# Optimization experiments

Measured on AMD Instinct MI355X. Metric: run time of the kernel, lower is better.

Reference implementation:

```python
import jax, jax.numpy as jnp
import numpy as np

EPS = 1e-12
H = 256
W = 256
RANK = 4
CTX = 1024
BATCH = 32
FF = (H + W) * RANK * 4  # 8192
STD = 0.001


def _norm(x, axis):
    # torch: (x - mean) / sqrt(var(unbiased) + eps)
    m = jnp.mean(x, axis=axis, keepdims=True)
    v = jnp.var(x, axis=axis, keepdims=True, ddof=1)
    return (x - m) / jnp.sqrt(v + EPS)


def _norm_polar(x):
    # x: [B, N, 2]; magnitude-normalize relative to per-batch max magnitude
    x_abs = jnp.sqrt(x[..., 0] ** 2 + x[..., 1] ** 2 + EPS)          # [B, N]
    h = x_abs / (jnp.max(x_abs, axis=-1, keepdims=True) + EPS)       # [B, N]
    xn = x / (x_abs[..., None] + EPS)                                # [B, N, 2]
    return jnp.stack([h * xn[..., 0], h * xn[..., 1]], axis=-1)


def setup_inputs() -> dict:
    key = jax.random.key(0)
    ks = jax.random.split(key, 12)

    def lin(k, fan_in, shape):
        b = 1.0 / np.sqrt(fan_in)
        return jax.random.uniform(k, shape, jnp.float32, -b, b)

    weights_static = jnp.concatenate([
        jax.random.normal(ks[9], (1, H, W, 2), jnp.float32) * STD,
        jax.random.normal(ks[10], (1, H, W, 2), jnp.float32) * STD
        + jnp.array([1.0, 0.0], jnp.float32),
    ], axis=0)  # [2, H, W, 2]

    return {
        "x": jax.random.normal(ks[0], (BATCH, CTX), jnp.float32),
        "W_in": lin(ks[1], CTX, (FF, CTX)),
        "b_in": lin(ks[2], CTX, (FF,)),
        "W_gate": lin(ks[3], CTX, (FF, CTX)),
        "b_gate": lin(ks[4], CTX, (FF,)),
        "W_t": lin(ks[5], FF, (FF, FF)),
        "b_t": lin(ks[6], FF, (FF,)),
        "conv_w": lin(ks[7], RANK, (RANK, RANK)),  # 1x1 conv kernel [out, in]
        "conv_b": lin(ks[8], RANK, (RANK,)),
        "weights_static": weights_static,
        "weights_mod": jax.random.normal(ks[11], (4, H, W), jnp.float32) * STD,
    }


def reference(x, W_in, b_in, W_gate, b_gate, W_t, b_t, conv_w, conv_b,
              weights_static, weights_mod):
    b = x.shape[0]
    # dual linear projections (dropout p=0 -> identity)
    xt = x @ W_in.T + b_in            # [B, FF]
    xg = x @ W_gate.T + b_gate        # [B, FF]
    stack = jnp.stack([xt, xg], axis=0).reshape(2, b, 4, -1)
    stack = _norm(stack, -1)
    ctx = (stack[0] * jnp.tanh(stack[1])).reshape(b, -1)   # gated, [B, FF]
    ctx = ctx @ W_t.T + b_t                                 # [B, FF]
    ctx = ctx.reshape(b, 4, RANK, H + W)
    modc = _norm(ctx, -1)
    # outer product -> [B, 4, RANK, H, W]
    mod = jnp.tanh(jnp.einsum('bkri,bkrj->bkrij', modc[..., :H], modc[..., H:]))
    # channel 0: 1x1 conv over rank channels, then sum channels (keepdim)
    mod_real = jnp.einsum('oi,bihw->bohw', conv_w, mod[:, 0]) + conv_b[None, :, None, None]
    mod_real = jnp.sum(mod_real, axis=1, keepdims=True)     # [B, 1, H, W]
    mod_other = jnp.sum(mod[:, 1:], axis=2)                 # [B, 3, H, W]
    mod = jnp.concatenate([mod_real, mod_other], axis=1)    # [B, 4, H, W]
    mod = weights_mod[None] * mod

    A0 = weights_static[0]            # [H, W, 2]
    A1 = weights_static[1]            # [H, W, 2]
    Bm = jnp.moveaxis(mod[:, 0:2], 1, -1)                   # [B, H, W, 2]
    ms_r = A1[..., 0] * Bm[..., 0] - A1[..., 1] * Bm[..., 1]
    ms_i = A1[..., 0] * Bm[..., 1] - A1[..., 1] * Bm[..., 0]
    mod_scaled = jnp.stack([ms_r, ms_i], axis=-1)           # [B, H, W, 2]
    mod_scaled = _norm_polar(mod_scaled.reshape(b, H * W, 2)).reshape(b, H, W, 2)

    mag = jnp.sqrt(mod_scaled[..., 0] ** 2 + mod_scaled[..., 1] ** 2 + EPS)
    mag = jnp.sqrt(jnp.mean(mag, axis=(-1, -2)) + EPS)      # [B]
    mod_scaled = mod_scaled / mag[:, None, None, None]

    mod_weights = A0[None] + mod_scaled                     # [B, H, W, 2]

    mod_proj = jnp.moveaxis(mod[:, 2:], 1, -1)              # [B, H, W, 2]
    mod_proj = _norm_polar(mod_proj.reshape(b, H * W, 2)).reshape(b, H, W, 2)
    den = jnp.sqrt(mod_proj[..., 0] ** 2 + mod_proj[..., 1] ** 2 + EPS)
    theta_cos = mod_proj[..., 0] / den
    theta_sin = mod_proj[..., 1] / den
    weights = mod_weights[..., 0] * theta_cos + mod_weights[..., 1] * theta_sin
    return weights  # [B, H, W]
```

## Files before the change

### kernel.cpp

```cpp
#include <hip/hip_runtime.h>
#include <cstddef>

#define NB   32
#define CTXD 1024
#define FFD  8192
#define HD   256
#define WD   256
#define NPIX 65536
#define EPSF 1e-12f

typedef __attribute__((ext_vector_type(8))) short bf16x8;
typedef __attribute__((ext_vector_type(4))) float f32x4;


__device__ __forceinline__ float ftanh(float x){
  float ax = fabsf(x);
  float e  = __expf(2.0f*ax);
  float r  = 1.0f - 2.0f*__builtin_amdgcn_rcpf(e + 1.0f);
  return copysignf(r, x);
}

__device__ __forceinline__ unsigned short f2bf(float f){
  unsigned u = __float_as_uint(f);
  unsigned r = (u + 0x7FFFu + ((u >> 16) & 1u)) >> 16;
  return (unsigned short)r;
}
__device__ __forceinline__ float bf2f(unsigned short s){
  return __uint_as_float((unsigned)s << 16);
}

__device__ __forceinline__ void split3(float f, unsigned short& s0,
                                       unsigned short& s1, unsigned short& s2){
  s0 = f2bf(f);
  float r1 = f - bf2f(s0);
  s1 = f2bf(r1);
  float r2 = r1 - bf2f(s1);
  s2 = f2bf(r2);
}

__device__ __forceinline__ void block_reduce4(float& a, float& b, float& c, float& d){
  for (int off = 32; off > 0; off >>= 1){
    a += __shfl_down(a, off); b += __shfl_down(b, off);
    c += __shfl_down(c, off); d += __shfl_down(d, off);
  }
  __shared__ float lds[16];
  int wid = threadIdx.x >> 6, lane = threadIdx.x & 63;
  if (lane == 0){ lds[wid*4+0]=a; lds[wid*4+1]=b; lds[wid*4+2]=c; lds[wid*4+3]=d; }
  __syncthreads();
  a = (lds[0]+lds[4])+(lds[8]+lds[12]);
  b = (lds[1]+lds[5])+(lds[9]+lds[13]);
  c = (lds[2]+lds[6])+(lds[10]+lds[14]);
  d = (lds[3]+lds[7])+(lds[11]+lds[15]);
}

__device__ __forceinline__ void pixel_core(
    const float* __restrict__ lds, int h, int w, int pix,
    float cw0, float cw1, float cw2, float cw3, float cb,
    const float* __restrict__ wmod, const float* __restrict__ wstat,
    float& r_, float& i_, float& p_, float& q_){
  float sk[4];
  #pragma unroll
  for (int k = 0; k < 4; ++k){
    float acc = 0.f;
    #pragma unroll
    for (int r = 0; r < 4; ++r){
      int kr = k*4 + r;
      float u  = lds[kr*512 + h];
      float vv = lds[kr*512 + 256 + w];
      float tt = ftanh(u*vv);
      float cwr = (r==0)?cw0:(r==1)?cw1:(r==2)?cw2:cw3;
      acc += (k==0) ? cwr*tt : tt;
    }
    sk[k] = acc;
  }
  sk[0] += cb;
  float m0 = sk[0]*wmod[0*NPIX+pix];
  float m1 = sk[1]*wmod[1*NPIX+pix];
  float m2 = sk[2]*wmod[2*NPIX+pix];
  float m3 = sk[3]*wmod[3*NPIX+pix];
  float2 A1 = *(const float2*)(wstat + (size_t)(NPIX + pix)*2);
  r_ = A1.x*m0 - A1.y*m1;
  i_ = A1.x*m1 - A1.y*m0;
  p_ = m2; q_ = m3;
}


__global__ __launch_bounds__(256) void k_prep(
    const float* __restrict__ x, unsigned short* __restrict__ P,
    float* __restrict__ red){
  int g = blockIdx.x*256 + threadIdx.x;
  if (g < 64) red[g] = 0.0f;
  int b = g >> 7, grp = g & 127;
  int koff = grp*8;
  int c = grp >> 2, kg = grp & 3;
  const float* src = x + (size_t)b*CTXD + koff;
  float4 v0 = *(const float4*)(src), v1 = *(const float4*)(src+4);
  float vv[8] = {v0.x,v0.y,v0.z,v0.w,v1.x,v1.y,v1.z,v1.w};
  bf16x8 a0, a1, a2;
  #pragma unroll
  for (int e = 0; e < 8; ++e){
    unsigned short s0,s1,s2; split3(vv[e],s0,s1,s2);
    a0[e]=(short)s0; a1[e]=(short)s1; a2[e]=(short)s2;
  }
  size_t base = (size_t)c*3072 + (b>>4)*512 + kg*128 + (b&15)*8;
  *(bf16x8*)(P + base)        = a0;
  *(bf16x8*)(P + base + 1024) = a1;
  *(bf16x8*)(P + base + 2048) = a2;
}

template<int KC>
__global__ __launch_bounds__(256) void k_gemm_mfma(
    const float* __restrict__ W0, const float* __restrict__ W1,
    const unsigned short* __restrict__ BP,
    float* __restrict__ Cp, int K, size_t zstride){
  const float* __restrict__ W = blockIdx.z ? W1 : W0;
  int wave = threadIdx.x >> 6;
  int lane = threadIdx.x & 63;
  int f0   = blockIdx.x*64 + wave*16;
  int kc   = blockIdx.y;
  int row  = lane & 15;
  int kg   = lane >> 4;
  int rot  = blockIdx.x & (KC-1);
  const float* Wb = W + (size_t)(f0+row)*K + kc*KC*32 + kg*8;
  const unsigned short* Bb = BP + (size_t)kc*KC*3072 + kg*128 + row*8;
  f32x4 acc0={0.f,0.f,0.f,0.f}, acc1={0.f,0.f,0.f,0.f};
  const float* wp = Wb + rot*32;
  float4 w0 = *(const float4*)(wp), w1 = *(const float4*)(wp+4);
  for (int c = 0; c < KC; ++c){
    int rc = (c + rot) & (KC-1);
    const unsigned short* bp = Bb + (size_t)rc*3072;
    bf16x8 b0h0 = *(const bf16x8*)(bp);
    bf16x8 b0h1 = *(const bf16x8*)(bp +  512);
    bf16x8 b1h0 = *(const bf16x8*)(bp + 1024);
    bf16x8 b1h1 = *(const bf16x8*)(bp + 1536);
    bf16x8 b2h0 = *(const bf16x8*)(bp + 2048);
    bf16x8 b2h1 = *(const bf16x8*)(bp + 2560);
    float4 cw0 = w0, cw1 = w1;
    if (c + 1 < KC){
      int rn = (c + 1 + rot) & (KC-1);
      wp = Wb + rn*32;
      w0 = *(const float4*)(wp); w1 = *(const float4*)(wp+4);
    }
    bf16x8 a0, a1, a2;
    float wv[8] = {cw0.x,cw0.y,cw0.z,cw0.w,cw1.x,cw1.y,cw1.z,cw1.w};
    #pragma unroll
    for (int e = 0; e < 8; ++e){
      unsigned short s0,s1,s2; split3(wv[e],s0,s1,s2);
      a0[e]=(short)s0; a1[e]=(short)s1; a2[e]=(short)s2;
    }
    acc0 = __builtin_amdgcn_mfma_f32_16x16x32_bf16(a0, b0h0, acc0, 0,0,0);
    acc1 = __builtin_amdgcn_mfma_f32_16x16x32_bf16(a0, b0h1, acc1, 0,0,0);
    acc0 = __builtin_amdgcn_mfma_f32_16x16x32_bf16(a0, b1h0, acc0, 0,0,0);
    acc1 = __builtin_amdgcn_mfma_f32_16x16x32_bf16(a0, b1h1, acc1, 0,0,0);
    acc0 = __builtin_amdgcn_mfma_f32_16x16x32_bf16(a1, b0h0, acc0, 0,0,0);
    acc1 = __builtin_amdgcn_mfma_f32_16x16x32_bf16(a1, b0h1, acc1, 0,0,0);
    acc0 = __builtin_amdgcn_mfma_f32_16x16x32_bf16(a0, b2h0, acc0, 0,0,0);
    acc1 = __builtin_amdgcn_mfma_f32_16x16x32_bf16(a0, b2h1, acc1, 0,0,0);
    acc0 = __builtin_amdgcn_mfma_f32_16x16x32_bf16(a1, b1h0, acc0, 0,0,0);
    acc1 = __builtin_amdgcn_mfma_f32_16x16x32_bf16(a1, b1h1, acc1, 0,0,0);
    acc0 = __builtin_amdgcn_mfma_f32_16x16x32_bf16(a2, b0h0, acc0, 0,0,0);
    acc1 = __builtin_amdgcn_mfma_f32_16x16x32_bf16(a2, b0h1, acc1, 0,0,0);
  }
  float* __restrict__ C = Cp + (size_t)blockIdx.z*zstride + (size_t)kc*(FFD*32);
  #pragma unroll
  for (int r = 0; r < 4; ++r){
    int f = f0 + kg*4 + r;
    C[(size_t)f*32 + row]      = acc0[r];
    C[(size_t)f*32 + 16 + row] = acc1[r];
  }
}

__global__ __launch_bounds__(256) void k_reduce1(
    const float* __restrict__ Cp, const float* __restrict__ bin,
    const float* __restrict__ bg, float* __restrict__ xtT,
    float* __restrict__ xgT){
  int g = blockIdx.x*256 + threadIdx.x;
  int m = g >> 18, idx = g & 262143;
  int f = idx >> 5;
  const float* __restrict__ cp = Cp + (size_t)m*(8ull*FFD*32);
  float s = (m ? bg : bin)[f];
  #pragma unroll
  for (int sI = 0; sI < 8; ++sI) s += cp[(size_t)sI*(FFD*32) + idx];
  (m ? xgT : xtT)[idx] = s;
}

__global__ __launch_bounds__(256) void k_reduce2(
    const float* __restrict__ Cp, const float* __restrict__ bias,
    float* __restrict__ outT){
  int g = blockIdx.x*256 + threadIdx.x;
  int f = g >> 5;
  float s = bias[f];
  #pragma unroll
  for (int sI = 0; sI < 16; ++sI) s += Cp[(size_t)sI*(FFD*32) + g];
  outT[g] = s;
}

__global__ __launch_bounds__(256) void k_normgate(
    const float* __restrict__ xtT, const float* __restrict__ xgT,
    unsigned short* __restrict__ P){
  int b = blockIdx.x >> 2, g4 = blockIdx.x & 3;
  int t = threadIdx.x;
  int f8 = g4*2048 + t*8;
  float vt[8], vg[8];
  float st=0.f, sst=0.f, sg=0.f, ssg=0.f;
  #pragma unroll
  for (int i = 0; i < 8; ++i){
    int f = f8 + i;
    float a = xtT[(size_t)f*NB + b];
    float c = xgT[(size_t)f*NB + b];
    vt[i]=a; vg[i]=c;
    st += a; sst += a*a; sg += c; ssg += c*c;
  }
  block_reduce4(st, sst, sg, ssg);
  float mt = st * (1.0f/2048.0f);
  float it = rsqrtf((sst - st*mt) * (1.0f/2047.0f) + EPSF);
  float mg = sg * (1.0f/2048.0f);
  float ig = rsqrtf((ssg - sg*mg) * (1.0f/2047.0f) + EPSF);
  bf16x8 a0, a1, a2;
  #pragma unroll
  for (int i = 0; i < 8; ++i){
    float nt = (vt[i]-mt)*it;
    float ng = (vg[i]-mg)*ig;
    float cv = nt * ftanh(ng);
    unsigned short s0,s1,s2; split3(cv,s0,s1,s2);
    a0[i]=(short)s0; a1[i]=(short)s1; a2[i]=(short)s2;
  }
  int c2 = f8 >> 5, kg = (f8 >> 3) & 3;
  size_t base = (size_t)c2*3072 + (b>>4)*512 + kg*128 + (b&15)*8;
  *(bf16x8*)(P + base)        = a0;
  *(bf16x8*)(P + base + 1024) = a1;
  *(bf16x8*)(P + base + 2048) = a2;
}

__global__ __launch_bounds__(256) void k_norm512(
    const float* __restrict__ ctx2T, float* __restrict__ modc){
  int b = blockIdx.x >> 4, kr = blockIdx.x & 15;
  int t = threadIdx.x;
  int base = kr*512;
  float v0 = ctx2T[(base + t      )*NB + b];
  float v1 = ctx2T[(base + 256 + t)*NB + b];
  float s = v0+v1, ss = v0*v0 + v1*v1, d0=0.f, d1=0.f;
  block_reduce4(s, ss, d0, d1);
  float m   = s * (1.0f/512.0f);
  float inv = rsqrtf((ss - s*m) * (1.0f/511.0f) + EPSF);
  modc[b*FFD + base + t      ] = (v0-m)*inv;
  modc[b*FFD + base + 256 + t] = (v1-m)*inv;
}

__global__ __launch_bounds__(256) void k_scan(
    const float* __restrict__ modc,
    const float* __restrict__ convw, const float* __restrict__ convb,
    const float* __restrict__ wmod, const float* __restrict__ wstat,
    float* __restrict__ red, float* __restrict__ magpart){
  int b = blockIdx.x >> 4, chunk = blockIdx.x & 15;
  int t = threadIdx.x;
  __shared__ float lds[16*512];
  #pragma unroll
  for (int i = 0; i < 8; ++i){
    float4 v = *(const float4*)(modc + (size_t)b*FFD + (i*256 + t)*4);
    *(float4*)(lds + (i*256 + t)*4) = v;
  }
  float cw0 = convw[0]+convw[4]+convw[8]+convw[12];
  float cw1 = convw[1]+convw[5]+convw[9]+convw[13];
  float cw2 = convw[2]+convw[6]+convw[10]+convw[14];
  float cw3 = convw[3]+convw[7]+convw[11]+convw[15];
  float cb  = convb[0]+convb[1]+convb[2]+convb[3];
  __syncthreads();
  int w = t;
  float mxs = 0.f, mxp = 0.f, sas = 0.f;
  for (int it = 0; it < 16; ++it){
    int h = chunk*16 + it;
    int pix = h*WD + w;
    float r_, i_, p_, q_;
    pixel_core(lds, h, w, pix, cw0, cw1, cw2, cw3, cb, wmod, wstat,
               r_, i_, p_, q_);
    float as = sqrtf(r_*r_ + i_*i_ + EPSF);
    float ap = sqrtf(p_*p_ + q_*q_ + EPSF);
    mxs = fmaxf(mxs, as); mxp = fmaxf(mxp, ap);
    sas += as;
  }
  for (int off = 32; off > 0; off >>= 1){
    mxs = fmaxf(mxs, __shfl_down(mxs, off));
    mxp = fmaxf(mxp, __shfl_down(mxp, off));
    sas += __shfl_down(sas, off);
  }
  __shared__ float lred[12];
  int wid = t >> 6, lane = t & 63;
  if (lane == 0){ lred[wid] = mxs; lred[4+wid] = mxp; lred[8+wid] = sas; }
  __syncthreads();
  if (t == 0){
    float a = fmaxf(fmaxf(lred[0],lred[1]), fmaxf(lred[2],lred[3]));
    float p = fmaxf(fmaxf(lred[4],lred[5]), fmaxf(lred[6],lred[7]));
    float s = (lred[8]+lred[9])+(lred[10]+lred[11]);
    atomicMax((int*)&red[b],    __float_as_int(a));
    atomicMax((int*)&red[32+b], __float_as_int(p));
    magpart[b*16 + chunk] = s;
  }
}

__global__ __launch_bounds__(256) void k_final(
    const float* __restrict__ modc,
    const float* __restrict__ convw, const float* __restrict__ convb,
    const float* __restrict__ wmod, const float* __restrict__ wstat,
    const float* __restrict__ red, const float* __restrict__ magpart,
    float* __restrict__ out){
  int b = blockIdx.x >> 4, chunk = blockIdx.x & 15;
  int t = threadIdx.x;
  __shared__ float lds[16*512];
  __shared__ float s_im;
  if (t < 16){
    float v = magpart[b*16 + t];
    for (int off = 8; off > 0; off >>= 1) v += __shfl_down(v, off);
    if (t == 0){
      float maxs = red[b];
      s_im = rsqrtf(v*(1.0f/65536.0f)/(maxs + EPSF) + EPSF);
    }
  }
  #pragma unroll
  for (int i = 0; i < 8; ++i){
    float4 v = *(const float4*)(modc + (size_t)b*FFD + (i*256 + t)*4);
    *(float4*)(lds + (i*256 + t)*4) = v;
  }
  float cw0 = convw[0]+convw[4]+convw[8]+convw[12];
  float cw1 = convw[1]+convw[5]+convw[9]+convw[13];
  float cw2 = convw[2]+convw[6]+convw[10]+convw[14];
  float cw3 = convw[3]+convw[7]+convw[11]+convw[15];
  float cb  = convb[0]+convb[1]+convb[2]+convb[3];
  __syncthreads();
  float im = s_im;
  float maxs = red[b], maxp = red[32+b];
  int w = t;
  for (int it = 0; it < 16; ++it){
    int h = chunk*16 + it;
    int pix = h*WD + w;
    float r_, i_, p_, q_;
    pixel_core(lds, h, w, pix, cw0, cw1, cw2, cw3, cb, wmod, wstat,
               r_, i_, p_, q_);
    float as = sqrtf(r_*r_ + i_*i_ + EPSF);
    float fs = (as/(maxs+EPSF))/(as+EPSF)*im;
    float2 A0 = *(const float2*)(wstat + (size_t)pix*2);
    float mwr = A0.x + fs*r_;
    float mwi = A0.y + fs*i_;
    float ap = sqrtf(p_*p_ + q_*q_ + EPSF);
    float fp = (ap/(maxp+EPSF))/(ap+EPSF);
    float mpr = fp*p_, mpi = fp*q_;
    float den = sqrtf(mpr*mpr + mpi*mpi + EPSF);
    out[(size_t)b*NPIX + pix] = (mwr*mpr + mwi*mpi)/den;
  }
}


extern "C" void kernel_launch(void* const* d_in, const int* in_sizes, int n_in,
                              void* d_out, int out_size, void* d_ws, size_t ws_size,
                              hipStream_t stream){
  const float* x     = (const float*)d_in[0];
  const float* Win   = (const float*)d_in[1];
  const float* bin   = (const float*)d_in[2];
  const float* Wg    = (const float*)d_in[3];
  const float* bg    = (const float*)d_in[4];
  const float* Wt    = (const float*)d_in[5];
  const float* bt    = (const float*)d_in[6];
  const float* convw = (const float*)d_in[7];
  const float* convb = (const float*)d_in[8];
  const float* wstat = (const float*)d_in[9];
  const float* wmod  = (const float*)d_in[10];
  float* out = (float*)d_out;
  float* ws  = (float*)d_ws;

  float* xtT   = ws;
  float* xgT   = ws + 262144;
  float* ctx2T = ws;
  float* modc  = ws + 262144;
  unsigned short* P2 = (unsigned short*)(ws + 524288);
  unsigned short* P1 = (unsigned short*)(ws + 917504);
  float* Cp    = ws + 966656;
  float* red     = ws + 5160960;
  float* magpart = ws + 5161024;

  k_prep<<<16, 256, 0, stream>>>(x, P1, red);
  k_gemm_mfma<4><<<dim3(128,8,2), 256, 0, stream>>>(Win, Wg, P1,
                                                    Cp, CTXD, 8ull*FFD*32);
  k_reduce1<<<2048, 256, 0, stream>>>(Cp, bin, bg, xtT, xgT);
  k_normgate<<<128, 256, 0, stream>>>(xtT, xgT, P2);
  k_gemm_mfma<16><<<dim3(128,16,1), 256, 0, stream>>>(Wt, Wt, P2,
                                                      Cp, FFD, 0);
  k_reduce2<<<1024, 256, 0, stream>>>(Cp, bt, ctx2T);
  k_norm512<<<512, 256, 0, stream>>>(ctx2T, modc);
  k_scan<<<512, 256, 0, stream>>>(modc, convw, convb, wmod, wstat, red, magpart);
  k_final<<<512, 256, 0, stream>>>(modc, convw, convb, wmod, wstat, red,
                                   magpart, out);
}
```

Before: 174.0 us.

## Stage W_t tiles via async global-to-LDS loads with double buffering

Replaces the direct-load MFMA GEMM for the large FFxFF projection with a new kernel. It streams 64x64 fp32 weight tiles into shared memory using the global_load_lds builtin, double-buffered so the next tile loads while the current one is split into three bf16 parts and fed to MFMA. The K-step order is rotated per block so neighbouring blocks read different column slices at the same time. This aims to hide DRAM latency on the bandwidth-bound weight stream, at the cost of 32KB of LDS per block and a barrier every step.

New measurement: 163.5 us. 6.0% less time.

```diff
diff --git a/kernel.cpp b/kernel.cpp
--- a/kernel.cpp
+++ b/kernel.cpp
@@ -36,6 +36,12 @@
   s1 = f2bf(r1);
   float r2 = r1 - bf2f(s1);
   s2 = f2bf(r2);
+}
+
+__device__ __forceinline__ void gload_lds16(const float* g, float* l){
+  __builtin_amdgcn_global_load_lds(
+      (__attribute__((address_space(1))) void*)const_cast<float*>(g),
+      (__attribute__((address_space(3))) void*)l, 16, 0, 0);
 }
 
 __device__ __forceinline__ void block_reduce4(float& a, float& b, float& c, float& d){
@@ -170,6 +176,94 @@
   }
 }
 
+template<int STEPS>
+__global__ __launch_bounds__(256) void k_gemm_lds(
+    const float* __restrict__ W, const unsigned short* __restrict__ BP,
+    float* __restrict__ Cp, int K){
+  __shared__ float tile[2][4096];
+  const int t    = threadIdx.x;
+  const int wv   = t >> 6, lane = t & 63;
+  const int f0   = blockIdx.x * 64;
+  const int kc   = blockIdx.y;
+  const int row  = lane & 15, kg = lane >> 4;
+  const int srot = blockIdx.x & (STEPS - 1);
+  const size_t kslice = (size_t)kc * STEPS * 64;
+
+  f32x4 acc0 = {0.f,0.f,0.f,0.f}, acc1 = {0.f,0.f,0.f,0.f};
+
+  auto stage = [&](int buf, int s){
+    const size_t kbase = kslice + (size_t)s*64;
+    #pragma unroll
+    for (int i = 0; i < 4; ++i){
+      int r = wv*16 + i*4 + (lane >> 4);
+      const float* gsrc = W + (size_t)(f0 + r)*K + kbase + (lane & 15)*4;
+      gload_lds16(gsrc, &tile[buf][(wv*16 + i*4)*64]);
+    }
+  };
+
+  int cur = 0;
+  stage(0, srot);
+  __syncthreads();
+
+  for (int s = 0; s < STEPS; ++s){
+    const int sc = (s + srot) & (STEPS - 1);
+    const int k0 = kc*STEPS*2 + sc*2;
+    const unsigned short* bp0 = BP + (size_t)k0*3072     + kg*128 + row*8;
+    const unsigned short* bp1 = BP + (size_t)(k0+1)*3072 + kg*128 + row*8;
+    bf16x8 c0b0h0 = *(const bf16x8*)(bp0);
+    bf16x8 c0b0h1 = *(const bf16x8*)(bp0 +  512);
+    bf16x8 c0b1h0 = *(const bf16x8*)(bp0 + 1024);
+    bf16x8 c0b1h1 = *(const bf16x8*)(bp0 + 1536);
+    bf16x8 c0b2h0 = *(const bf16x8*)(bp0 + 2048);
+    bf16x8 c0b2h1 = *(const bf16x8*)(bp0 + 2560);
+    bf16x8 c1b0h0 = *(const bf16x8*)(bp1);
+    bf16x8 c1b0h1 = *(const bf16x8*)(bp1 +  512);
+    bf16x8 c1b1h0 = *(const bf16x8*)(bp1 + 1024);
+    bf16x8 c1b1h1 = *(const bf16x8*)(bp1 + 1536);
+    bf16x8 c1b2h0 = *(const bf16x8*)(bp1 + 2048);
+    bf16x8 c1b2h1 = *(const bf16x8*)(bp1 + 2560);
+    if (s + 1 < STEPS) stage(cur ^ 1, (s + 1 + srot) & (STEPS - 1));
+    #pragma unroll
+    for (int c = 0; c < 2; ++c){
+      const float* wp = &tile[cur][(wv*16 + row)*64 + c*32 + kg*8];
+      float4 w0 = *(const float4*)(wp);
+      float4 w1 = *(const float4*)(wp + 4);
+      bf16x8 a0, a1, a2;
+      float wv8[8] = {w0.x,w0.y,w0.z,w0.w,w1.x,w1.y,w1.z,w1.w};
+      #pragma unroll
+      for (int e = 0; e < 8; ++e){
+        unsigned short s0,s1,s2; split3(wv8[e],s0,s1,s2);
+        a0[e]=(short)s0; a1[e]=(short)s1; a2[e]=(short)s2;
+      }
+      bf16x8 b0h0 = c ? c1b0h0 : c0b0h0, b0h1 = c ? c1b0h1 : c0b0h1;
+      bf16x8 b1h0 = c ? c1b1h0 : c0b1h0, b1h1 = c ? c1b1h1 : c0b1h1;
+      bf16x8 b2h0 = c ? c1b2h0 : c0b2h0, b2h1 = c ? c1b2h1 : c0b2h1;
+      acc0 = __builtin_amdgcn_mfma_f32_16x16x32_bf16(a0, b0h0, acc0, 0,0,0);
+      acc1 = __builtin_amdgcn_mfma_f32_16x16x32_bf16(a0, b0h1, acc1, 0,0,0);
+      acc0 = __builtin_amdgcn_mfma_f32_16x16x32_bf16(a0, b1h0, acc0, 0,0,0);
+      acc1 = __builtin_amdgcn_mfma_f32_16x16x32_bf16(a0, b1h1, acc1, 0,0,0);
+      acc0 = __builtin_amdgcn_mfma_f32_16x16x32_bf16(a1, b0h0, acc0, 0,0,0);
+      acc1 = __builtin_amdgcn_mfma_f32_16x16x32_bf16(a1, b0h1, acc1, 0,0,0);
+      acc0 = __builtin_amdgcn_mfma_f32_16x16x32_bf16(a0, b2h0, acc0, 0,0,0);
+      acc1 = __builtin_amdgcn_mfma_f32_16x16x32_bf16(a0, b2h1, acc1, 0,0,0);
+      acc0 = __builtin_amdgcn_mfma_f32_16x16x32_bf16(a1, b1h0, acc0, 0,0,0);
+      acc1 = __builtin_amdgcn_mfma_f32_16x16x32_bf16(a1, b1h1, acc1, 0,0,0);
+      acc0 = __builtin_amdgcn_mfma_f32_16x16x32_bf16(a2, b0h0, acc0, 0,0,0);
+      acc1 = __builtin_amdgcn_mfma_f32_16x16x32_bf16(a2, b0h1, acc1, 0,0,0);
+    }
+    __syncthreads();
+    cur ^= 1;
+  }
+
+  float* __restrict__ C = Cp + (size_t)kc*(FFD*32);
+  #pragma unroll
+  for (int r = 0; r < 4; ++r){
+    int f = f0 + wv*16 + kg*4 + r;
+    C[(size_t)f*32 + row]      = acc0[r];
+    C[(size_t)f*32 + 16 + row] = acc1[r];
+  }
+}
+
 __global__ __launch_bounds__(256) void k_reduce1(
     const float* __restrict__ Cp, const float* __restrict__ bin,
     const float* __restrict__ bg, float* __restrict__ xtT,
@@ -382,8 +476,7 @@
                                                     Cp, CTXD, 8ull*FFD*32);
   k_reduce1<<<2048, 256, 0, stream>>>(Cp, bin, bg, xtT, xgT);
   k_normgate<<<128, 256, 0, stream>>>(xtT, xgT, P2);
-  k_gemm_mfma<16><<<dim3(128,16,1), 256, 0, stream>>>(Wt, Wt, P2,
-                                                      Cp, FFD, 0);
+  k_gemm_lds<8><<<dim3(128,16), 256, 0, stream>>>(Wt, P2, Cp, FFD);
   k_reduce2<<<1024, 256, 0, stream>>>(Cp, bt, ctx2T);
   k_norm512<<<512, 256, 0, stream>>>(ctx2T, modc);
   k_scan<<<512, 256, 0, stream>>>(modc, convw, convb, wmod, wstat, red, magpart);
```
